# Kernel tuning notes

Measured on AMD Instinct MI355X. Metric: run time of the kernel, lower is better.

Reference implementation:

```python
import jax, jax.numpy as jnp
import numpy as np

T, B, D = 2048, 32, 1024


def setup_inputs() -> dict:
    key = jax.random.key(0)
    k1, k2, k3 = jax.random.split(key, 3)
    x = jax.random.normal(k1, (T, B, D), dtype=jnp.float32)
    h0 = jnp.zeros((B, D), dtype=jnp.float32)
    # xavier-uniform-ish init: std ~= sqrt(2/(fan_in+fan_out)) = sqrt(1/D); W_h uses gain 0.5
    std = (1.0 / D) ** 0.5
    W_x = jax.random.normal(k2, (D, D), dtype=jnp.float32) * std
    W_h = jax.random.normal(k3, (D, D), dtype=jnp.float32) * (0.5 * std)
    b = jnp.zeros((D,), dtype=jnp.float32)
    return {"x": x, "h0": h0, "W_x": W_x, "W_h": W_h, "b": b}


def reference(x, h0, W_x, W_h, b):
    # h_t = tanh(x_t @ W_x + h_{t-1} @ W_h + b)   (haste stock-elman layout)
    # Precompute the input projection for all timesteps in one big GEMM.
    xW = jnp.einsum('tbd,de->tbe', x, W_x) + b  # [T, B, D]

    def step(h_prev, xw_t):
        h_new = jnp.tanh(xw_t + h_prev @ W_h)
        return h_new, h_new

    _, hs = jax.lax.scan(step, h0, xW)  # hs: [T, B, D]
    h_all = jnp.concatenate([h0[None], hs], axis=0)  # [T+1, B, D]
    return hs, h_all
```

## Files before the change

### kernel.cpp

```cpp
#include <hip/hip_runtime.h>
#include <hip/hip_fp16.h>

#define T_STEPS 2048
#define BATCH   32
#define DIM     1024
#define NWG     32
#define WCOLS   32

typedef _Float16 half2_t __attribute__((ext_vector_type(2)));
typedef _Float16 f16x4 __attribute__((ext_vector_type(4)));
typedef _Float16 f16x8 __attribute__((ext_vector_type(8)));
typedef float    f32x4 __attribute__((ext_vector_type(4)));

__device__ __forceinline__ f16x8 cvt8(f32x4 a, f32x4 b) {
    f16x8 r;
    r[0]=(_Float16)a[0]; r[1]=(_Float16)a[1]; r[2]=(_Float16)a[2]; r[3]=(_Float16)a[3];
    r[4]=(_Float16)b[0]; r[5]=(_Float16)b[1]; r[6]=(_Float16)b[2]; r[7]=(_Float16)b[3];
    return r;
}

__global__ void flag_init(int* __restrict__ f) { f[threadIdx.x] = 0; }

__global__ void conv_pack(const float* __restrict__ Wh, _Float16* __restrict__ P) {
    const int idx = blockIdx.x * blockDim.x + threadIdx.x;
    const int k = idx >> 10, n = idx & (DIM - 1);
    const int pos = (k >> 3) ^ (n & 7);
    P[(size_t)n * 1024 + pos * 8 + (k & 7)] = (_Float16)Wh[idx];
}

#define BM 128
#define BN 128
#define BK 32
#define LDT 40

__global__ __launch_bounds__(256) void gemm_xw(
    const float* __restrict__ X, const float* __restrict__ Wx,
    const float* __restrict__ bias, float* __restrict__ out)
{
    __shared__ _Float16 As[BM][LDT];
    __shared__ _Float16 Bs[BN][LDT];

    const int tid = threadIdx.x;
    const int m0 = blockIdx.x * BM, n0 = blockIdx.y * BN;
    const int lane = tid & 63, wid = tid >> 6;
    const int wm = (wid >> 1) * 64, wn = (wid & 1) * 64;
    const int lr = lane & 15, lk = (lane >> 4) * 8;
    const int ar = tid >> 1, ac = (tid & 1) * 16;
    const int bk = tid >> 3, bn = (tid & 7) * 16;

    f32x4 acc[4][4] = {};

    for (int k0 = 0; k0 < DIM; k0 += BK) {
        __syncthreads();
        {
            const float* src = X + (size_t)(m0 + ar) * DIM + k0 + ac;
            float4 q0 = *(const float4*)(src + 0);
            float4 q1 = *(const float4*)(src + 4);
            float4 q2 = *(const float4*)(src + 8);
            float4 q3 = *(const float4*)(src + 12);
            f16x8 p0, p1;
            p0[0]=(_Float16)q0.x; p0[1]=(_Float16)q0.y; p0[2]=(_Float16)q0.z; p0[3]=(_Float16)q0.w;
            p0[4]=(_Float16)q1.x; p0[5]=(_Float16)q1.y; p0[6]=(_Float16)q1.z; p0[7]=(_Float16)q1.w;
            p1[0]=(_Float16)q2.x; p1[1]=(_Float16)q2.y; p1[2]=(_Float16)q2.z; p1[3]=(_Float16)q2.w;
            p1[4]=(_Float16)q3.x; p1[5]=(_Float16)q3.y; p1[6]=(_Float16)q3.z; p1[7]=(_Float16)q3.w;
            *(f16x8*)&As[ar][ac] = p0;
            *(f16x8*)&As[ar][ac + 8] = p1;
        }
        {
            const float* src = Wx + (size_t)(k0 + bk) * DIM + n0 + bn;
            float4 q0 = *(const float4*)(src + 0);
            float4 q1 = *(const float4*)(src + 4);
            float4 q2 = *(const float4*)(src + 8);
            float4 q3 = *(const float4*)(src + 12);
            float vv[16];
            *(float4*)&vv[0] = q0; *(float4*)&vv[4] = q1;
            *(float4*)&vv[8] = q2; *(float4*)&vv[12] = q3;
            #pragma unroll
            for (int i = 0; i < 16; ++i) Bs[bn + i][bk] = (_Float16)vv[i];
        }
        __syncthreads();
        f16x8 a[4], bb[4];
        #pragma unroll
        for (int f = 0; f < 4; ++f) a[f]  = *(const f16x8*)&As[wm + f * 16 + lr][lk];
        #pragma unroll
        for (int f = 0; f < 4; ++f) bb[f] = *(const f16x8*)&Bs[wn + f * 16 + lr][lk];
        #pragma unroll
        for (int i = 0; i < 4; ++i)
            #pragma unroll
            for (int j = 0; j < 4; ++j)
                acc[i][j] = __builtin_amdgcn_mfma_f32_16x16x32_f16(a[i], bb[j], acc[i][j], 0, 0, 0);
    }

    #pragma unroll
    for (int i = 0; i < 4; ++i)
        #pragma unroll
        for (int j = 0; j < 4; ++j) {
            const int col = n0 + wn + j * 16 + lr;
            const float bv = bias[col];
            #pragma unroll
            for (int r = 0; r < 4; ++r) {
                const int row = m0 + wm + i * 16 + (lane >> 4) * 4 + r;
                __builtin_nontemporal_store(acc[i][j][r] + bv, out + (size_t)row * DIM + col);
            }
        }
}

__global__ __launch_bounds__(256, 1) void elman_rec(
    const float* __restrict__ h0, const _Float16* __restrict__ P,
    float* __restrict__ hs, float* __restrict__ h_all,
    int* __restrict__ flags, _Float16* __restrict__ xchg)
{
    __shared__ _Float16 Hs[32 * 128 * 8];
    __shared__ _Float16 Ws[32 * 128 * 8];
    __shared__ _Float16 ht2h[2 * 4 * 32 * 36];

    const int wg  = blockIdx.x;
    const int tid = threadIdx.x;
    const int w = tid >> 6, lane = tid & 63, lr = lane & 15, kg = lane >> 4;
    const int wcol0 = wg * WCOLS;

    {
        const uint4* src = (const uint4*)(P + (size_t)wcol0 * 1024);
        uint4* dst = (uint4*)Ws;
        #pragma unroll
        for (int j = 0; j < 16; ++j) dst[tid + 256 * j] = src[tid + 256 * j];
    }
    #pragma unroll
    for (int j = 0; j < 16; ++j) {
        const int bi = tid + 256 * j;
        const int r = bi >> 7, blk = bi & 127;
        f32x4 q0 = *(const f32x4*)(h0 + (size_t)r * DIM + blk * 8);
        f32x4 q1 = *(const f32x4*)(h0 + (size_t)r * DIM + blk * 8 + 4);
        *(f16x8*)&Hs[((r << 7) + (blk ^ (r & 7))) * 8] = cvt8(q0, q1);
        if (wg == 0) {
            *(f32x4*)(h_all + (size_t)r * DIM + blk * 8)     = q0;
            *(f32x4*)(h_all + (size_t)r * DIM + blk * 8 + 4) = q1;
        }
    }
    __syncthreads();

    const int er = tid >> 3, ec4 = (tid & 7) * 4;
    const int rl_rh = lane >> 5;
    const int rl_blk = 32 * w + (lane & 31);

    for (int t = 0; t < T_STEPS; ++t) {
        float* slot = h_all + (size_t)(t + 1) * (BATCH * DIM);
        f32x4 xw = *(const f32x4*)(slot + (size_t)er * DIM + wcol0 + ec4);

        f32x4 a00 = {0,0,0,0}, a01 = {0,0,0,0}, a10 = {0,0,0,0}, a11 = {0,0,0,0};
        #pragma unroll
        for (int q = 0; q < 8; ++q) {
            const int blk = (w * 8 + q) * 4 + kg;
            const int pa = blk ^ (lr & 7);
            f16x8 A0 = *(const f16x8*)&Hs[((lr << 7) + pa) * 8];
            f16x8 A1 = *(const f16x8*)&Hs[(((16 + lr) << 7) + pa) * 8];
            f16x8 B0 = *(const f16x8*)&Ws[((lr << 7) + pa) * 8];
            f16x8 B1 = *(const f16x8*)&Ws[(((16 + lr) << 7) + pa) * 8];
            a00 = __builtin_amdgcn_mfma_f32_16x16x32_f16(A0, B0, a00, 0, 0, 0);
            a01 = __builtin_amdgcn_mfma_f32_16x16x32_f16(A0, B1, a01, 0, 0, 0);
            a10 = __builtin_amdgcn_mfma_f32_16x16x32_f16(A1, B0, a10, 0, 0, 0);
            a11 = __builtin_amdgcn_mfma_f32_16x16x32_f16(A1, B1, a11, 0, 0, 0);
        }
        {
            _Float16* hb = ht2h + (size_t)(t & 1) * (4 * 32 * 36) + (size_t)w * (32 * 36);
            #pragma unroll
            for (int r = 0; r < 4; ++r) {
                hb[(kg * 4 + r) * 36 + lr]           = (_Float16)a00[r];
                hb[(kg * 4 + r) * 36 + 16 + lr]      = (_Float16)a01[r];
                hb[(16 + kg * 4 + r) * 36 + lr]      = (_Float16)a10[r];
                hb[(16 + kg * 4 + r) * 36 + 16 + lr] = (_Float16)a11[r];
            }
        }
        __syncthreads();

        f32x4 z = xw;
        {
            const _Float16* hb = ht2h + (size_t)(t & 1) * (4 * 32 * 36);
            #pragma unroll
            for (int ww = 0; ww < 4; ++ww) {
                f16x4 pv = *(const f16x4*)&hb[(ww * 32 + er) * 36 + ec4];
                z[0] += (float)pv[0]; z[1] += (float)pv[1];
                z[2] += (float)pv[2]; z[3] += (float)pv[3];
            }
        }
        f32x4 h;
        #pragma unroll
        for (int i = 0; i < 4; ++i) {
            const float e = __expf(2.0f * z[i]);
            h[i] = 1.0f - 2.0f / (e + 1.0f);
        }

        if (t == T_STEPS - 1) {
            __builtin_nontemporal_store(h, (f32x4*)(hs + (size_t)t * (BATCH * DIM)
                                                    + (size_t)er * DIM + wcol0 + ec4));
            *(f32x4*)(slot + (size_t)er * DIM + wcol0 + ec4) = h;
            break;
        }

        {
            half2_t lo, hi;
            lo[0] = (_Float16)h[0]; lo[1] = (_Float16)h[1];
            hi[0] = (_Float16)h[2]; hi[1] = (_Float16)h[3];
            uint2 pk;
            pk.x = __builtin_bit_cast(unsigned, lo);
            pk.y = __builtin_bit_cast(unsigned, hi);
            _Float16* xp = xchg + (size_t)((t + 1) & 1) * (BATCH * DIM)
                         + (size_t)er * DIM + wcol0 + ec4;
            asm volatile("global_store_dwordx2 %0, %1, off sc1"
                         :: "v"(xp), "v"(pk) : "memory");
        }
        asm volatile("s_waitcnt vmcnt(0)" ::: "memory");
        if (lane == 0)
            __hip_atomic_store(flags + (wg * 4 + w) * 4, t + 1,
                               __ATOMIC_RELAXED, __HIP_MEMORY_SCOPE_AGENT);

        if (lane < 32) {
            const int* fp = flags + ((8 * w + (lane >> 2)) * 4 + (lane & 3)) * 4;
            int g = 0, v;
            do {
                v = __hip_atomic_load(fp, __ATOMIC_RELAXED, __HIP_MEMORY_SCOPE_AGENT);
            } while (v < t + 1 && ++g < (1 << 20));
        }

        const _Float16* xb = xchg + (size_t)((t + 1) & 1) * (BATCH * DIM);
        uint4 q[16];
        #pragma unroll
        for (int i = 0; i < 16; ++i) {
            const int row = 2 * i + rl_rh;
            const _Float16* ap = xb + (size_t)row * DIM + rl_blk * 8;
            asm volatile("global_load_dwordx4 %0, %1, off sc1"
                         : "=v"(q[i]) : "v"(ap) : "memory");
        }
        asm volatile("s_waitcnt vmcnt(0)" ::: "memory");
        __builtin_amdgcn_sched_barrier(0);
        #pragma unroll
        for (int i = 0; i < 16; ++i) {
            const int row = 2 * i + rl_rh;
            *(uint4*)&Hs[((row << 7) + (rl_blk ^ (row & 7))) * 8] = q[i];
        }

        __builtin_nontemporal_store(h, (f32x4*)(hs + (size_t)t * (BATCH * DIM)
                                                + (size_t)er * DIM + wcol0 + ec4));
        *(f32x4*)(slot + (size_t)er * DIM + wcol0 + ec4) = h;
    }
}

extern "C" void kernel_launch(void* const* d_in, const int* in_sizes, int n_in,
                              void* d_out, int out_size, void* d_ws, size_t ws_size,
                              hipStream_t stream) {
    const float* x    = (const float*)d_in[0];
    const float* h0   = (const float*)d_in[1];
    const float* Wx   = (const float*)d_in[2];
    const float* Wh   = (const float*)d_in[3];
    const float* bias = (const float*)d_in[4];

    float* hs    = (float*)d_out;
    float* h_all = hs + (size_t)T_STEPS * BATCH * DIM;

    int*       flags = (int*)d_ws;
    _Float16*  xchg  = (_Float16*)((char*)d_ws + 4096);
    _Float16*  P     = (_Float16*)((char*)d_ws + 4096 + 131072);

    flag_init<<<1, 1024, 0, stream>>>((int*)d_ws);
    conv_pack<<<(DIM * DIM) / 256, 256, 0, stream>>>(Wh, P);

    dim3 g((T_STEPS * BATCH) / BM, DIM / BN);
    gemm_xw<<<g, 256, 0, stream>>>(x, Wx, bias, h_all + (size_t)BATCH * DIM);

    elman_rec<<<NWG, 256, 0, stream>>>(h0, P, hs, h_all, flags, xchg);
}
```

Before: 8.367 ms.

## Replace per-step flag barrier with tagged data exchange and lagged reuse flags

The per-step exchange of fp16 hidden state between workgroups no longer stores, drains, sets a flag and then spins on flags. Instead, each packed word carries a 3-cycle tag in the low mantissa bits, and readers poll the data itself until every tag matches, reloading only rows that are still missing. A separate 'read done' flag, checked two steps later, guards reuse of the double-buffered exchange slot. The aim is to take one full global round trip off the critical path each step. The cost is that tag bits overwrite mantissa LSBs of the fp16 values, and stale-tag aliasing with the 3-value tag needs care to stay correct.

Result: slower. 9.252 ms (+10.6%).

```diff
diff --git a/kernel.cpp b/kernel.cpp
--- a/kernel.cpp
+++ b/kernel.cpp
@@ -12,6 +12,8 @@
 typedef _Float16 f16x8 __attribute__((ext_vector_type(8)));
 typedef float    f32x4 __attribute__((ext_vector_type(4)));
 
+#define TAG_MASK 0x00010001u
+
 __device__ __forceinline__ f16x8 cvt8(f32x4 a, f32x4 b) {
     f16x8 r;
     r[0]=(_Float16)a[0]; r[1]=(_Float16)a[1]; r[2]=(_Float16)a[2]; r[3]=(_Float16)a[3];
@@ -20,6 +22,11 @@
 }
 
 __global__ void flag_init(int* __restrict__ f) { f[threadIdx.x] = 0; }
+
+__global__ void ring_scrub(uint2* __restrict__ ring) {
+    const int i = blockIdx.x * blockDim.x + threadIdx.x;
+    ring[i] = uint2{TAG_MASK, TAG_MASK};
+}
 
 __global__ void conv_pack(const float* __restrict__ Wh, _Float16* __restrict__ P) {
     const int idx = blockIdx.x * blockDim.x + threadIdx.x;
@@ -108,7 +115,7 @@
 __global__ __launch_bounds__(256, 1) void elman_rec(
     const float* __restrict__ h0, const _Float16* __restrict__ P,
     float* __restrict__ hs, float* __restrict__ h_all,
-    int* __restrict__ flags, _Float16* __restrict__ xchg)
+    int* __restrict__ rdone, _Float16* __restrict__ xchg)
 {
     __shared__ _Float16 Hs[32 * 128 * 8];
     __shared__ _Float16 Ws[32 * 128 * 8];
@@ -142,6 +149,9 @@
     const int er = tid >> 3, ec4 = (tid & 7) * 4;
     const int rl_rh = lane >> 5;
     const int rl_blk = 32 * w + (lane & 31);
+    const int cw = wg >> 3;
+
+    int tag = 1;
 
     for (int t = 0; t < T_STEPS; ++t) {
         float* slot = h_all + (size_t)(t + 1) * (BATCH * DIM);
@@ -171,6 +181,14 @@
                 hb[(16 + kg * 4 + r) * 36 + 16 + lr] = (_Float16)a11[r];
             }
         }
+
+        if (w == 0 && lane < 32 && t >= 2) {
+            const int* fp = rdone + ((lane * 4 + cw) * 4);
+            int g = 0, v;
+            do {
+                v = __hip_atomic_load(fp, __ATOMIC_RELAXED, __HIP_MEMORY_SCOPE_AGENT);
+            } while (v < t - 1 && ++g < (1 << 20));
+        }
         __syncthreads();
 
         f32x4 z = xw;
@@ -191,47 +209,51 @@
         }
 
         if (t == T_STEPS - 1) {
-            __builtin_nontemporal_store(h, (f32x4*)(hs + (size_t)t * (BATCH * DIM)
-                                                    + (size_t)er * DIM + wcol0 + ec4));
+            *(f32x4*)(hs + (size_t)t * (BATCH * DIM) + (size_t)er * DIM + wcol0 + ec4) = h;
             *(f32x4*)(slot + (size_t)er * DIM + wcol0 + ec4) = h;
             break;
         }
+
+        const unsigned exp_pat = (unsigned)(tag & 1) | ((unsigned)(tag >> 1) << 16);
 
         {
             half2_t lo, hi;
             lo[0] = (_Float16)h[0]; lo[1] = (_Float16)h[1];
             hi[0] = (_Float16)h[2]; hi[1] = (_Float16)h[3];
             uint2 pk;
-            pk.x = __builtin_bit_cast(unsigned, lo);
+            pk.x = (__builtin_bit_cast(unsigned, lo) & ~TAG_MASK) | exp_pat;
             pk.y = __builtin_bit_cast(unsigned, hi);
             _Float16* xp = xchg + (size_t)((t + 1) & 1) * (BATCH * DIM)
                          + (size_t)er * DIM + wcol0 + ec4;
             asm volatile("global_store_dwordx2 %0, %1, off sc1"
                          :: "v"(xp), "v"(pk) : "memory");
         }
-        asm volatile("s_waitcnt vmcnt(0)" ::: "memory");
-        if (lane == 0)
-            __hip_atomic_store(flags + (wg * 4 + w) * 4, t + 1,
-                               __ATOMIC_RELAXED, __HIP_MEMORY_SCOPE_AGENT);
-
-        if (lane < 32) {
-            const int* fp = flags + ((8 * w + (lane >> 2)) * 4 + (lane & 3)) * 4;
-            int g = 0, v;
-            do {
-                v = __hip_atomic_load(fp, __ATOMIC_RELAXED, __HIP_MEMORY_SCOPE_AGENT);
-            } while (v < t + 1 && ++g < (1 << 20));
-        }
+        *(f32x4*)(hs + (size_t)t * (BATCH * DIM) + (size_t)er * DIM + wcol0 + ec4) = h;
+        *(f32x4*)(slot + (size_t)er * DIM + wcol0 + ec4) = h;
 
         const _Float16* xb = xchg + (size_t)((t + 1) & 1) * (BATCH * DIM);
         uint4 q[16];
-        #pragma unroll
-        for (int i = 0; i < 16; ++i) {
-            const int row = 2 * i + rl_rh;
-            const _Float16* ap = xb + (size_t)row * DIM + rl_blk * 8;
-            asm volatile("global_load_dwordx4 %0, %1, off sc1"
-                         : "=v"(q[i]) : "v"(ap) : "memory");
-        }
-        asm volatile("s_waitcnt vmcnt(0)" ::: "memory");
+        unsigned need = 0xFFFFu;
+        int g = 0;
+        do {
+            #pragma unroll
+            for (int i = 0; i < 16; ++i) {
+                if (need & (1u << i)) {
+                    const int row = 2 * i + rl_rh;
+                    const _Float16* ap = xb + (size_t)row * DIM + rl_blk * 8;
+                    asm volatile("global_load_dwordx4 %0, %1, off sc1"
+                                 : "=v"(q[i]) : "v"(ap) : "memory");
+                }
+            }
+            asm volatile("s_waitcnt vmcnt(0)" ::: "memory");
+            #pragma unroll
+            for (int i = 0; i < 16; ++i) {
+                if (need & (1u << i)) {
+                    const unsigned bad = ((q[i].x ^ exp_pat) | (q[i].z ^ exp_pat)) & TAG_MASK;
+                    if (bad == 0) need &= ~(1u << i);
+                }
+            }
+        } while (need && ++g < (1 << 20));
         __builtin_amdgcn_sched_barrier(0);
         #pragma unroll
         for (int i = 0; i < 16; ++i) {
@@ -239,9 +261,11 @@
             *(uint4*)&Hs[((row << 7) + (rl_blk ^ (row & 7))) * 8] = q[i];
         }
 
-        __builtin_nontemporal_store(h, (f32x4*)(hs + (size_t)t * (BATCH * DIM)
-                                                + (size_t)er * DIM + wcol0 + ec4));
-        *(f32x4*)(slot + (size_t)er * DIM + wcol0 + ec4) = h;
+        if (lane == 0)
+            __hip_atomic_store(rdone + ((wg * 4 + w) * 4), t + 1,
+                               __ATOMIC_RELAXED, __HIP_MEMORY_SCOPE_AGENT);
+
+        tag = (tag == 2) ? 0 : tag + 1;
     }
 }
 
@@ -257,15 +281,16 @@
     float* hs    = (float*)d_out;
     float* h_all = hs + (size_t)T_STEPS * BATCH * DIM;
 
-    int*       flags = (int*)d_ws;
+    int*       rdone = (int*)d_ws;
     _Float16*  xchg  = (_Float16*)((char*)d_ws + 4096);
     _Float16*  P     = (_Float16*)((char*)d_ws + 4096 + 131072);
 
     flag_init<<<1, 1024, 0, stream>>>((int*)d_ws);
+    ring_scrub<<<64, 256, 0, stream>>>((uint2*)xchg);
     conv_pack<<<(DIM * DIM) / 256, 256, 0, stream>>>(Wh, P);
 
     dim3 g((T_STEPS * BATCH) / BM, DIM / BN);
     gemm_xw<<<g, 256, 0, stream>>>(x, Wx, bias, h_all + (size_t)BATCH * DIM);
 
-    elman_rec<<<NWG, 256, 0, stream>>>(h0, P, hs, h_all, flags, xchg);
-}
+    elman_rec<<<NWG, 256, 0, stream>>>(h0, P, hs, h_all, rdone, xchg);
+}
```
